# Kernel optimization log

Hardware: AMD Instinct MI355X
Metric: run time of the kernel (lower is better)

## Reference

```python
import jax, jax.numpy as jnp
import numpy as np
import math

N_NODES = 100000
N_EDGES = 1600000
IN_FEATS = 64
H_FEATS = 64
NUM_CLASSES = 2
LS_D = [2, 4, 6, 8]
LS_COEFF = [1.0, 1.0, 1.0, 1.0]
K = 4  # polynomial order per conv (len of each theta)


def _chi_theta(d, coeff):
    # Faithful port of calculate_theta_Chi for d > 0: fit chi-square-like
    # density on [0,2] with a degree-3 Chebyshev series, reverse coeffs.
    n = 2 * d
    m = 1.0 / (n / 2 + 1)  # i = n/2 - 1, m = 1/(i+2)
    def y(x):
        x = np.asarray(x, dtype=np.float64)
        return 1.0 / (2 ** (n / 2) * math.gamma(n / 2)) * (x / m) ** (n / 2 - 1) * np.exp(-(x / m) / 2)
    xs = np.linspace(0.0, 2.0, 20001)
    S = np.trapz(y(xs), xs)  # dense trapezoid ~ scipy.integrate.quad on [0,2]
    lambs = np.linspace(0.0, 2.0, 500)
    c = np.polynomial.chebyshev.chebfit(lambs, y(lambs) / S, 3)
    return (c[::-1] * coeff).astype(np.float32)

THETAS_NP = np.stack([_chi_theta(d, c) for d, c in zip(LS_D, LS_COEFF)])  # [4, K]


def setup_inputs() -> dict:
    key = jax.random.key(0)
    ks = jax.random.split(key, 8)
    sc = 0.05
    return {
        "x": jax.random.normal(ks[0], (N_NODES, IN_FEATS), dtype=jnp.float32),
        "src": jax.random.randint(ks[1], (N_EDGES,), 0, N_NODES, dtype=jnp.int32),
        "dst": jax.random.randint(ks[2], (N_EDGES,), 0, N_NODES, dtype=jnp.int32),
        "thetas": jnp.asarray(THETAS_NP),
        "W1": jax.random.normal(ks[3], (IN_FEATS, H_FEATS), dtype=jnp.float32) * sc,
        "b1": jnp.zeros((H_FEATS,), dtype=jnp.float32),
        "W2": jax.random.normal(ks[4], (H_FEATS, H_FEATS), dtype=jnp.float32) * sc,
        "b2": jnp.zeros((H_FEATS,), dtype=jnp.float32),
        "Wm1": jax.random.normal(ks[5], (H_FEATS * len(LS_D), H_FEATS), dtype=jnp.float32) * sc,
        "bm1": jnp.zeros((H_FEATS,), dtype=jnp.float32),
        "Wm2": jax.random.normal(ks[6], (H_FEATS, NUM_CLASSES), dtype=jnp.float32) * sc,
        "bm2": jnp.zeros((NUM_CLASSES,), dtype=jnp.float32),
    }


def reference(x, src, dst, thetas, W1, b1, W2, b2, Wm1, bm1, Wm2, bm2):
    n = x.shape[0]
    # input MLP stem
    h = jax.nn.relu(x @ W1 + b1)
    h = jax.nn.relu(h @ W2 + b2)
    # D^{-1/2} from in-degrees (clamped to >= 1), as in DGL in_degrees()
    deg = jax.ops.segment_sum(jnp.ones_like(dst, dtype=h.dtype), dst, num_segments=n)
    dinv = jnp.maximum(deg, 1.0) ** -0.5  # [N]
    dinv = dinv[:, None]  # [N, 1]
    # shared Laplacian power sequence: feats[k] = L^k h with L = I - D^-1/2 A D^-1/2
    feats = [h]
    f = h
    for _ in range(K - 1):
        t = f * dinv                                   # [N, H]
        agg = jax.ops.segment_sum(t[src], dst, num_segments=n)  # gather-scatter SpMM
        f = f - agg * dinv
        feats.append(f)
    F = jnp.stack(feats)  # [K, N, H]
    # per-conv polynomial combination, then concat along feature dim
    h_final = jnp.einsum('ck,knh->nch', thetas, F).reshape(n, -1)  # [N, C*H]
    # output MLP (2 layers)
    h_out = jax.nn.relu(h_final @ Wm1 + bm1)
    return h_out @ Wm2 + bm2
```

## Files before the change

kernel.cpp:

```cpp
#include <hip/hip_runtime.h>
#include <math.h>

#define TS  256
#define GS  192
#define BCAP2 4608
#define CHUNK 4096

typedef __attribute__((ext_vector_type(8))) short short8v;
typedef __attribute__((ext_vector_type(4))) float f32x4;

__device__ __forceinline__ unsigned short f2bf(float f) {
    unsigned int u = __builtin_bit_cast(unsigned int, f);
    u += 0x7fff + ((u >> 16) & 1);
    return (unsigned short)(u >> 16);
}
__device__ __forceinline__ float bf2f(unsigned short s) {
    return __builtin_bit_cast(float, ((unsigned int)s) << 16);
}
__device__ __forceinline__ void fma4(float4& a, float s, const float4& b) {
    a.x = fmaf(s, b.x, a.x);
    a.y = fmaf(s, b.y, a.y);
    a.z = fmaf(s, b.z, a.z);
    a.w = fmaf(s, b.w, a.w);
}

__global__ void zero_k(int* __restrict__ p, int n) {
    int i = blockIdx.x * blockDim.x + threadIdx.x;
    int st = gridDim.x * blockDim.x;
    for (; i < n; i += st) p[i] = 0;
}

__global__ __launch_bounds__(256) void part1_k(const int* __restrict__ src,
        const int* __restrict__ dst, int* __restrict__ gcnt,
        unsigned int* __restrict__ pairs, int E, int NB) {
    __shared__ int lcnt[512];
    __shared__ int lbase[512];
    __shared__ int lpos[512];
    int tid = threadIdx.x;
    int base = blockIdx.x * CHUNK;
    int m = E - base; if (m > CHUNK) m = CHUNK;
    for (int b = tid; b < NB; b += 256) { lcnt[b] = 0; lpos[b] = 0; }
    __syncthreads();
    for (int i = tid; i < m; i += 256)
        atomicAdd(&lcnt[dst[base + i] >> 8], 1);
    __syncthreads();
    for (int b = tid; b < NB; b += 256)
        lbase[b] = (lcnt[b] > 0) ? atomicAdd(&gcnt[b], lcnt[b]) : 0;
    __syncthreads();
    for (int i = tid; i < m; i += 256) {
        int s = src[base + i], d = dst[base + i];
        int b = d >> 8;
        int p = atomicAdd(&lpos[b], 1);
        int idx = lbase[b] + p;
        if (idx < BCAP2)
            pairs[(size_t)b * BCAP2 + idx] = (unsigned int)s | ((unsigned int)(d & 255) << 17);
    }
}

__global__ __launch_bounds__(512) void bscan_k(const int* __restrict__ gcnt,
        int* __restrict__ bbase, int* __restrict__ rowp, int NB, int E, int n) {
    __shared__ int buf[512];
    int tid = threadIdx.x;
    int v = (tid < NB) ? (gcnt[tid] > BCAP2 ? BCAP2 : gcnt[tid]) : 0;
    buf[tid] = v;
    __syncthreads();
    int x = v;
    for (int off = 1; off < 512; off <<= 1) {
        int t = (tid >= off) ? buf[tid - off] : 0;
        __syncthreads();
        x += t;
        buf[tid] = x;
        __syncthreads();
    }
    if (tid < NB) bbase[tid] = x - v;
    if (tid == 0) rowp[n] = E;
}

__global__ __launch_bounds__(256) void csr2_k(const int* __restrict__ gcnt,
        const unsigned int* __restrict__ pairs, const int* __restrict__ bbase,
        int* __restrict__ rowp, int* __restrict__ colb, float* __restrict__ dinv, int n) {
    int b = blockIdx.x;
    int tid = threadIdx.x;
    int cntb = gcnt[b]; if (cntb > BCAP2) cntb = BCAP2;
    const unsigned int* pb = pairs + (size_t)b * BCAP2;
    __shared__ int c[256];
    __shared__ int sc[256];
    __shared__ int lpos[256];
    c[tid] = 0; lpos[tid] = 0;
    __syncthreads();
    for (int i = tid; i < cntb; i += 256)
        atomicAdd(&c[pb[i] >> 17], 1);
    __syncthreads();
    int v = c[tid];
    sc[tid] = v;
    __syncthreads();
    int x = v;
    for (int off = 1; off < 256; off <<= 1) {
        int t = (tid >= off) ? sc[tid - off] : 0;
        __syncthreads();
        x += t;
        sc[tid] = x;
        __syncthreads();
    }
    int ex = x - v;
    sc[tid] = ex;
    int node = b * 256 + tid;
    if (node < n) {
        rowp[node] = bbase[b] + ex;
        dinv[node] = 1.0f / sqrtf((float)(v > 1 ? v : 1));
    }
    __syncthreads();
    for (int i = tid; i < cntb; i += 256) {
        unsigned int pk = pb[i];
        int j = pk >> 17;
        int p = atomicAdd(&lpos[j], 1);
        colb[bbase[b] + sc[j] + p] = (int)(pk & 0x1FFFF);
    }
}

__global__ __launch_bounds__(256) void mlp_k(const float* __restrict__ x,
        const float* __restrict__ W1, const float* __restrict__ b1,
        const float* __restrict__ W2, const float* __restrict__ b2,
        const float* __restrict__ dinv,
        unsigned short* __restrict__ Ghi, unsigned short* __restrict__ Glo,
        int n, int ntiles) {
    __shared__ float Ws1[64 * 64];
    __shared__ float Ws2[64 * 64];
    __shared__ float xT[64 * 68];
    int tid = threadIdx.x;
    int ti = tid >> 4, tj = tid & 15;
    for (int idx = tid; idx < 4096; idx += 256) { Ws1[idx] = W1[idx]; Ws2[idx] = W2[idx]; }
    float4 b1v = *(const float4*)&b1[4 * tj];
    float4 b2v = *(const float4*)&b2[4 * tj];

    for (int g = blockIdx.x; g < ntiles; g += gridDim.x) {
        int base = g * 64;
        __syncthreads();
        for (int it = 0; it < 4; it++) {
            int node = ti + it * 16;
            int gn = base + node;
            float4 v = make_float4(0.f, 0.f, 0.f, 0.f);
            if (gn < n) v = *(const float4*)&x[(size_t)gn * 64 + 4 * tj];
            xT[(4 * tj + 0) * 68 + node] = v.x;
            xT[(4 * tj + 1) * 68 + node] = v.y;
            xT[(4 * tj + 2) * 68 + node] = v.z;
            xT[(4 * tj + 3) * 68 + node] = v.w;
        }
        __syncthreads();

        float4 a0 = b1v, a1 = b1v, a2 = b1v, a3 = b1v;
        #pragma unroll 8
        for (int k = 0; k < 64; k++) {
            float4 xv = *(const float4*)&xT[k * 68 + 4 * ti];
            float4 wv = *(const float4*)&Ws1[k * 64 + 4 * tj];
            fma4(a0, xv.x, wv); fma4(a1, xv.y, wv); fma4(a2, xv.z, wv); fma4(a3, xv.w, wv);
        }
        __syncthreads();
        {
            int hb = (4 * tj) * 68 + 4 * ti;
            xT[hb + 0 * 68 + 0] = fmaxf(a0.x, 0.f);
            xT[hb + 1 * 68 + 0] = fmaxf(a0.y, 0.f);
            xT[hb + 2 * 68 + 0] = fmaxf(a0.z, 0.f);
            xT[hb + 3 * 68 + 0] = fmaxf(a0.w, 0.f);
            xT[hb + 0 * 68 + 1] = fmaxf(a1.x, 0.f);
            xT[hb + 1 * 68 + 1] = fmaxf(a1.y, 0.f);
            xT[hb + 2 * 68 + 1] = fmaxf(a1.z, 0.f);
            xT[hb + 3 * 68 + 1] = fmaxf(a1.w, 0.f);
            xT[hb + 0 * 68 + 2] = fmaxf(a2.x, 0.f);
            xT[hb + 1 * 68 + 2] = fmaxf(a2.y, 0.f);
            xT[hb + 2 * 68 + 2] = fmaxf(a2.z, 0.f);
            xT[hb + 3 * 68 + 2] = fmaxf(a2.w, 0.f);
            xT[hb + 0 * 68 + 3] = fmaxf(a3.x, 0.f);
            xT[hb + 1 * 68 + 3] = fmaxf(a3.y, 0.f);
            xT[hb + 2 * 68 + 3] = fmaxf(a3.z, 0.f);
            xT[hb + 3 * 68 + 3] = fmaxf(a3.w, 0.f);
        }
        __syncthreads();

        a0 = b2v; a1 = b2v; a2 = b2v; a3 = b2v;
        #pragma unroll 8
        for (int k = 0; k < 64; k++) {
            float4 xv = *(const float4*)&xT[k * 68 + 4 * ti];
            float4 wv = *(const float4*)&Ws2[k * 64 + 4 * tj];
            fma4(a0, xv.x, wv); fma4(a1, xv.y, wv); fma4(a2, xv.z, wv); fma4(a3, xv.w, wv);
        }
        int gn0 = base + 4 * ti;
#define STORE_ROW(ai, ii)                                                                  \
        {                                                                                  \
            int gn = gn0 + (ii);                                                           \
            if (gn < n) {                                                                  \
                float dg = dinv[gn];                                                       \
                float g0 = fmaxf(ai.x, 0.f) * dg, g1 = fmaxf(ai.y, 0.f) * dg;              \
                float g2 = fmaxf(ai.z, 0.f) * dg, g3 = fmaxf(ai.w, 0.f) * dg;              \
                ushort4 hv, lv;                                                            \
                hv.x = f2bf(g0); lv.x = f2bf(g0 - bf2f(hv.x));                             \
                hv.y = f2bf(g1); lv.y = f2bf(g1 - bf2f(hv.y));                             \
                hv.z = f2bf(g2); lv.z = f2bf(g2 - bf2f(hv.z));                             \
                hv.w = f2bf(g3); lv.w = f2bf(g3 - bf2f(hv.w));                             \
                *(ushort4*)&Ghi[(size_t)gn * TS + 4 * tj] = hv;                            \
                *(ushort4*)&Glo[(size_t)gn * GS + 4 * tj] = lv;                            \
            }                                                                              \
        }
        STORE_ROW(a0, 0) STORE_ROW(a1, 1) STORE_ROW(a2, 2) STORE_ROW(a3, 3)
#undef STORE_ROW
    }
}

__global__ void wm1p_k(const float* __restrict__ thetas, const float* __restrict__ Wm1,
                       unsigned short* __restrict__ Wth, unsigned short* __restrict__ Wtl) {
    int idx = blockIdx.x * blockDim.x + threadIdx.x;
    if (idx >= 16384) return;
    int j = idx & 63;
    int q = idx >> 6;
    int k = q >> 6;
    int hh = q & 63;
    float a = 0.f;
    for (int c = 0; c < 4; c++) a += thetas[c * 4 + k] * Wm1[(c * 64 + hh) * 64 + j];
    unsigned short hi = f2bf(a);
    float r = a - bf2f(hi);
    Wth[j * 256 + q] = hi;
    Wtl[j * 256 + q] = f2bf(r);
}

__global__ __launch_bounds__(256) void prop_k(
        const unsigned short* __restrict__ TinHi,
        const unsigned short* __restrict__ TinLo,
        unsigned short* __restrict__ ToutHi,
        unsigned short* __restrict__ ToutLo,
        const int* __restrict__ rowp, const int* __restrict__ colb,
        const float* __restrict__ dinv, int n, int writeLo) {
    int w = (blockIdx.x * blockDim.x + threadIdx.x) >> 6;
    int lane = threadIdx.x & 63;
    int nA = 2 * w, nB = 2 * w + 1;
    if (nA >= n) return;
    bool hasB = (nB < n);
    int eA = rowp[nA], endA = rowp[nA + 1];
    int eB = 0, endB = 0;
    if (hasB) { eB = rowp[nB]; endB = rowp[nB + 1]; }
    float a0 = 0.f, a1 = 0.f, b0 = 0.f, b1 = 0.f;
    while (eA + 7 < endA && eB + 7 < endB) {
        int sA0 = colb[eA],     sA1 = colb[eA + 1], sA2 = colb[eA + 2], sA3 = colb[eA + 3];
        int sA4 = colb[eA + 4], sA5 = colb[eA + 5], sA6 = colb[eA + 6], sA7 = colb[eA + 7];
        int sB0 = colb[eB],     sB1 = colb[eB + 1], sB2 = colb[eB + 2], sB3 = colb[eB + 3];
        int sB4 = colb[eB + 4], sB5 = colb[eB + 5], sB6 = colb[eB + 6], sB7 = colb[eB + 7];
        float fA0 = bf2f(TinHi[(size_t)sA0 * TS + lane]);
        float fA1 = bf2f(TinHi[(size_t)sA1 * TS + lane]);
        float fA2 = bf2f(TinHi[(size_t)sA2 * TS + lane]);
        float fA3 = bf2f(TinHi[(size_t)sA3 * TS + lane]);
        float fA4 = bf2f(TinHi[(size_t)sA4 * TS + lane]);
        float fA5 = bf2f(TinHi[(size_t)sA5 * TS + lane]);
        float fA6 = bf2f(TinHi[(size_t)sA6 * TS + lane]);
        float fA7 = bf2f(TinHi[(size_t)sA7 * TS + lane]);
        float fB0 = bf2f(TinHi[(size_t)sB0 * TS + lane]);
        float fB1 = bf2f(TinHi[(size_t)sB1 * TS + lane]);
        float fB2 = bf2f(TinHi[(size_t)sB2 * TS + lane]);
        float fB3 = bf2f(TinHi[(size_t)sB3 * TS + lane]);
        float fB4 = bf2f(TinHi[(size_t)sB4 * TS + lane]);
        float fB5 = bf2f(TinHi[(size_t)sB5 * TS + lane]);
        float fB6 = bf2f(TinHi[(size_t)sB6 * TS + lane]);
        float fB7 = bf2f(TinHi[(size_t)sB7 * TS + lane]);
        a0 += (fA0 + fA2) + (fA4 + fA6);
        a1 += (fA1 + fA3) + (fA5 + fA7);
        b0 += (fB0 + fB2) + (fB4 + fB6);
        b1 += (fB1 + fB3) + (fB5 + fB7);
        eA += 8; eB += 8;
    }
    while (eA + 3 < endA) {
        int s0 = colb[eA], s1 = colb[eA + 1], s2 = colb[eA + 2], s3 = colb[eA + 3];
        float f0 = bf2f(TinHi[(size_t)s0 * TS + lane]);
        float f1 = bf2f(TinHi[(size_t)s1 * TS + lane]);
        float f2 = bf2f(TinHi[(size_t)s2 * TS + lane]);
        float f3 = bf2f(TinHi[(size_t)s3 * TS + lane]);
        a0 += f0 + f2; a1 += f1 + f3;
        eA += 4;
    }
    while (eB + 3 < endB) {
        int s0 = colb[eB], s1 = colb[eB + 1], s2 = colb[eB + 2], s3 = colb[eB + 3];
        float f0 = bf2f(TinHi[(size_t)s0 * TS + lane]);
        float f1 = bf2f(TinHi[(size_t)s1 * TS + lane]);
        float f2 = bf2f(TinHi[(size_t)s2 * TS + lane]);
        float f3 = bf2f(TinHi[(size_t)s3 * TS + lane]);
        b0 += f0 + f2; b1 += f1 + f3;
        eB += 4;
    }
    for (; eA < endA; ++eA) a0 += bf2f(TinHi[(size_t)colb[eA] * TS + lane]);
    for (; eB < endB; ++eB) b0 += bf2f(TinHi[(size_t)colb[eB] * TS + lane]);

    {
        float acc = a0 + a1;
        float dg = dinv[nA];
        float gin = bf2f(TinHi[(size_t)nA * TS + lane]) + bf2f(TinLo[(size_t)nA * GS + lane]);
        float go = gin - dg * dg * acc;
        unsigned short hi = f2bf(go);
        ToutHi[(size_t)nA * TS + lane] = hi;
        if (writeLo) ToutLo[(size_t)nA * GS + lane] = f2bf(go - bf2f(hi));
    }
    if (hasB) {
        float acc = b0 + b1;
        float dg = dinv[nB];
        float gin = bf2f(TinHi[(size_t)nB * TS + lane]) + bf2f(TinLo[(size_t)nB * GS + lane]);
        float go = gin - dg * dg * acc;
        unsigned short hi = f2bf(go);
        ToutHi[(size_t)nB * TS + lane] = hi;
        if (writeLo) ToutLo[(size_t)nB * GS + lane] = f2bf(go - bf2f(hi));
    }
}

__global__ __launch_bounds__(512) void final_k(const unsigned short* __restrict__ Ghi,
        const float* __restrict__ dinv,
        const unsigned short* __restrict__ Wth, const unsigned short* __restrict__ Wtl,
        const float* __restrict__ bm1, const float* __restrict__ Wm2,
        const float* __restrict__ bm2, float* __restrict__ out, int n, int ntiles) {
    __shared__ unsigned short Bs[32768];
    __shared__ unsigned short As[32768];
    __shared__ float Lp[4][128][2];
    int tid = threadIdx.x;
    int w = tid >> 6, l = tid & 63;
    int cw = w & 3, half = w >> 2;
    int colg = 16 * cw + (l & 15);
    int grp = l >> 4;

    for (int i = tid; i < 4096; i += 512) {
        int byte = i * 16;
        int col = byte >> 9;
        int swz = byte ^ ((col & 7) << 4);
        uint4 v = (byte < 32768) ? *(const uint4*)((const char*)Wth + byte)
                                 : *(const uint4*)((const char*)Wtl + (byte - 32768));
        *(uint4*)((char*)Bs + swz) = v;
    }
    float bm1c = bm1[colg];
    float w2x = Wm2[colg * 2 + 0], w2y = Wm2[colg * 2 + 1];
    float bo0 = bm2[0], bo1 = bm2[1];
    __syncthreads();

    for (int g = blockIdx.x; g < ntiles; g += gridDim.x) {
        const char* asrc = (const char*)(Ghi + (size_t)g * 128 * TS);
        for (int i = tid; i < 4096; i += 512) {
            int byte = i * 16;
            int row = byte >> 9;
            int swz = byte ^ ((row & 7) << 4);
            *(uint4*)((char*)As + swz) = *(const uint4*)(asrc + byte);
        }
        __syncthreads();

        for (int rt = 0; rt < 4; rt++) {
            int arow = half * 64 + rt * 16 + (l & 15);
            int abase = arow * 512 + grp * 16;
            int axor = (arow & 7) << 4;
            int bbase = colg * 512 + grp * 16;
            int bxor = (colg & 7) << 4;
            f32x4 acc = {0.f, 0.f, 0.f, 0.f};
            #pragma unroll
            for (int ks = 0; ks < 8; ks++) {
                short8v a  = *(const short8v*)((const char*)As + ((abase + ks * 64) ^ axor));
                int bb = (bbase + ks * 64) ^ bxor;
                short8v bh = *(const short8v*)((const char*)Bs + bb);
                short8v bl = *(const short8v*)((const char*)Bs + (bb + 32768));
                acc = __builtin_amdgcn_mfma_f32_16x16x32_bf16(a, bh, acc, 0, 0, 0);
                acc = __builtin_amdgcn_mfma_f32_16x16x32_bf16(a, bl, acc, 0, 0, 0);
            }
            #pragma unroll
            for (int i = 0; i < 4; i++) {
                int rl = half * 64 + rt * 16 + (l >> 4) * 4 + i;
                int grow = g * 128 + rl;
                float s = (grow < n) ? (1.0f / dinv[grow]) : 0.f;
                float h = fmaxf(fmaf(acc[i], s, bm1c), 0.f);
                float q0 = h * w2x, q1 = h * w2y;
                q0 += __shfl_xor(q0, 1); q1 += __shfl_xor(q1, 1);
                q0 += __shfl_xor(q0, 2); q1 += __shfl_xor(q1, 2);
                q0 += __shfl_xor(q0, 4); q1 += __shfl_xor(q1, 4);
                q0 += __shfl_xor(q0, 8); q1 += __shfl_xor(q1, 8);
                if ((l & 15) == 0) {
                    Lp[cw][rl][0] = q0;
                    Lp[cw][rl][1] = q1;
                }
            }
        }
        __syncthreads();
        if (tid < 256) {
            int r = tid >> 1, ch = tid & 1;
            int grow = g * 128 + r;
            if (grow < n) {
                float v = Lp[0][r][ch] + Lp[1][r][ch] + Lp[2][r][ch] + Lp[3][r][ch]
                        + ((ch == 0) ? bo0 : bo1);
                out[grow * 2 + ch] = v;
            }
        }
    }
}

extern "C" void kernel_launch(void* const* d_in, const int* in_sizes, int n_in,
                              void* d_out, int out_size, void* d_ws, size_t ws_size,
                              hipStream_t stream) {
    const float* x      = (const float*)d_in[0];
    const int*   src    = (const int*)d_in[1];
    const int*   dst    = (const int*)d_in[2];
    const float* thetas = (const float*)d_in[3];
    const float* W1     = (const float*)d_in[4];
    const float* b1     = (const float*)d_in[5];
    const float* W2     = (const float*)d_in[6];
    const float* b2     = (const float*)d_in[7];
    const float* Wm1    = (const float*)d_in[8];
    const float* bm1    = (const float*)d_in[9];
    const float* Wm2    = (const float*)d_in[10];
    const float* bm2    = (const float*)d_in[11];
    float* out = (float*)d_out;

    int n = in_sizes[0] / 64;
    int E = in_sizes[1];
    int ntiles  = (n + 63) / 64;
    int ntiles2 = (n + 127) / 128;
    int NB = (n + 255) / 256;

    unsigned short* Glo = (unsigned short*)d_ws;
    float* dinv  = (float*)(Glo + (size_t)n * GS);
    int*   rowp  = (int*)(dinv + n);
    int*   colb  = rowp + (n + 1);
    size_t woff = (((size_t)(colb + E) - (size_t)d_ws) + 15) & ~(size_t)15;
    unsigned short* Wth = (unsigned short*)((char*)d_ws + woff);
    unsigned short* Wtl = Wth + 16384;
    int*   gcnt  = (int*)(Wtl + 16384);
    int*   bbase = gcnt + NB;
    size_t uoff = (((size_t)(bbase + NB) - (size_t)d_ws) + 255) & ~(size_t)255;
    unsigned int*   pairs = (unsigned int*)((char*)d_ws + uoff);
    unsigned short* Ghi   = (unsigned short*)pairs;

    int nchunksP = (E + CHUNK - 1) / CHUNK;

    zero_k<<<4, 256, 0, stream>>>(gcnt, NB);
    part1_k<<<nchunksP, 256, 0, stream>>>(src, dst, gcnt, pairs, E, NB);
    bscan_k<<<1, 512, 0, stream>>>(gcnt, bbase, rowp, NB, E, n);
    csr2_k<<<NB, 256, 0, stream>>>(gcnt, pairs, bbase, rowp, colb, dinv, n);

    mlp_k<<<768, 256, 0, stream>>>(x, W1, b1, W2, b2, dinv, Ghi, Glo, n, ntiles);
    wm1p_k<<<64, 256, 0, stream>>>(thetas, Wm1, Wth, Wtl);

    int nwaves = (n + 1) / 2;
    int pblocks = ((size_t)nwaves * 64 + 255) / 256;
    prop_k<<<pblocks, 256, 0, stream>>>(
        Ghi + 0 * 64, Glo + 0 * 64, Ghi + 1 * 64, Glo + 1 * 64, rowp, colb, dinv, n, 1);
    prop_k<<<pblocks, 256, 0, stream>>>(
        Ghi + 1 * 64, Glo + 1 * 64, Ghi + 2 * 64, Glo + 2 * 64, rowp, colb, dinv, n, 1);
    prop_k<<<pblocks, 256, 0, stream>>>(
        Ghi + 2 * 64, Glo + 2 * 64, Ghi + 3 * 64, Glo + 2 * 64, rowp, colb, dinv, n, 0);

    int fgrid = ntiles2 < 256 ? ntiles2 : 256;
    final_k<<<fgrid, 512, 0, stream>>>(Ghi, dinv, Wth, Wtl, bm1, Wm2, bm2, out, n, ntiles2);
}
```

Measured before the change: 277.3 us.

## Use split-bf16 MFMA for input MLP and drop the bucket scan kernel

The input MLP moves from scalar FP32 FMAs in LDS to bf16 MFMA 16x16x32 with hi/lo split operands (three MFMAs per step), using swizzled LDS tiles and weights pre-transposed by the extended wm1p kernel. The bucket prefix-scan kernel is replaced by an atomic running total in csr2_k, so bucket order becomes arbitrary. rowp now packs the start offset and degree into one word, so prop_k reads one value per node instead of two. The zeroing kernel becomes a memset. The split-bf16 scheme drops the lo*lo term, which slightly changes precision.

```diff
diff --git a/kernel.cpp b/kernel.cpp
--- a/kernel.cpp
+++ b/kernel.cpp
@@ -16,18 +16,6 @@
 }
 __device__ __forceinline__ float bf2f(unsigned short s) {
     return __builtin_bit_cast(float, ((unsigned int)s) << 16);
-}
-__device__ __forceinline__ void fma4(float4& a, float s, const float4& b) {
-    a.x = fmaf(s, b.x, a.x);
-    a.y = fmaf(s, b.y, a.y);
-    a.z = fmaf(s, b.z, a.z);
-    a.w = fmaf(s, b.w, a.w);
-}
-
-__global__ void zero_k(int* __restrict__ p, int n) {
-    int i = blockIdx.x * blockDim.x + threadIdx.x;
-    int st = gridDim.x * blockDim.x;
-    for (; i < n; i += st) p[i] = 0;
 }
 
 __global__ __launch_bounds__(256) void part1_k(const int* __restrict__ src,
@@ -57,28 +45,10 @@
     }
 }
 
-__global__ __launch_bounds__(512) void bscan_k(const int* __restrict__ gcnt,
-        int* __restrict__ bbase, int* __restrict__ rowp, int NB, int E, int n) {
-    __shared__ int buf[512];
-    int tid = threadIdx.x;
-    int v = (tid < NB) ? (gcnt[tid] > BCAP2 ? BCAP2 : gcnt[tid]) : 0;
-    buf[tid] = v;
-    __syncthreads();
-    int x = v;
-    for (int off = 1; off < 512; off <<= 1) {
-        int t = (tid >= off) ? buf[tid - off] : 0;
-        __syncthreads();
-        x += t;
-        buf[tid] = x;
-        __syncthreads();
-    }
-    if (tid < NB) bbase[tid] = x - v;
-    if (tid == 0) rowp[n] = E;
-}
-
 __global__ __launch_bounds__(256) void csr2_k(const int* __restrict__ gcnt,
-        const unsigned int* __restrict__ pairs, const int* __restrict__ bbase,
-        int* __restrict__ rowp, int* __restrict__ colb, float* __restrict__ dinv, int n) {
+        int* __restrict__ gtot, const unsigned int* __restrict__ pairs,
+        unsigned int* __restrict__ rowp, int* __restrict__ colb,
+        float* __restrict__ dinv, int n) {
     int b = blockIdx.x;
     int tid = threadIdx.x;
     int cntb = gcnt[b]; if (cntb > BCAP2) cntb = BCAP2;
@@ -86,6 +56,8 @@
     __shared__ int c[256];
     __shared__ int sc[256];
     __shared__ int lpos[256];
+    __shared__ int sbase;
+    if (tid == 0) sbase = atomicAdd(gtot, cntb);
     c[tid] = 0; lpos[tid] = 0;
     __syncthreads();
     for (int i = tid; i < cntb; i += 256)
@@ -104,9 +76,10 @@
     }
     int ex = x - v;
     sc[tid] = ex;
+    int bbase = sbase;
     int node = b * 256 + tid;
     if (node < n) {
-        rowp[node] = bbase[b] + ex;
+        rowp[node] = (unsigned int)(bbase + ex) | ((unsigned int)v << 21);
         dinv[node] = 1.0f / sqrtf((float)(v > 1 ? v : 1));
     }
     __syncthreads();
@@ -114,112 +87,179 @@
         unsigned int pk = pb[i];
         int j = pk >> 17;
         int p = atomicAdd(&lpos[j], 1);
-        colb[bbase[b] + sc[j] + p] = (int)(pk & 0x1FFFF);
+        colb[bbase + sc[j] + p] = (int)(pk & 0x1FFFF);
+    }
+}
+
+__global__ void wm1p_k(const float* __restrict__ thetas, const float* __restrict__ Wm1,
+                       const float* __restrict__ W1, const float* __restrict__ W2,
+                       unsigned short* __restrict__ Wth, unsigned short* __restrict__ Wtl,
+                       unsigned short* __restrict__ W1th, unsigned short* __restrict__ W1tl,
+                       unsigned short* __restrict__ W2th, unsigned short* __restrict__ W2tl) {
+    int idx = blockIdx.x * blockDim.x + threadIdx.x;
+    if (idx < 16384) {
+        int j = idx & 63;
+        int q = idx >> 6;
+        int k = q >> 6;
+        int hh = q & 63;
+        float a = 0.f;
+        for (int c = 0; c < 4; c++) a += thetas[c * 4 + k] * Wm1[(c * 64 + hh) * 64 + j];
+        unsigned short hi = f2bf(a);
+        Wth[j * 256 + q] = hi;
+        Wtl[j * 256 + q] = f2bf(a - bf2f(hi));
+    } else if (idx < 24576) {
+        int t = idx - 16384;
+        const float* W = (t < 4096) ? W1 : W2;
+        unsigned short* Th = (t < 4096) ? W1th : W2th;
+        unsigned short* Tl = (t < 4096) ? W1tl : W2tl;
+        int u = t & 4095;
+        int j = u >> 6, k = u & 63;
+        float a = W[k * 64 + j];
+        unsigned short hi = f2bf(a);
+        Th[u] = hi;
+        Tl[u] = f2bf(a - bf2f(hi));
     }
 }
 
 __global__ __launch_bounds__(256) void mlp_k(const float* __restrict__ x,
-        const float* __restrict__ W1, const float* __restrict__ b1,
-        const float* __restrict__ W2, const float* __restrict__ b2,
+        const unsigned short* __restrict__ W1th, const unsigned short* __restrict__ W1tl,
+        const unsigned short* __restrict__ W2th, const unsigned short* __restrict__ W2tl,
+        const float* __restrict__ b1, const float* __restrict__ b2,
         const float* __restrict__ dinv,
         unsigned short* __restrict__ Ghi, unsigned short* __restrict__ Glo,
         int n, int ntiles) {
-    __shared__ float Ws1[64 * 64];
-    __shared__ float Ws2[64 * 64];
-    __shared__ float xT[64 * 68];
+    __shared__ __align__(16) unsigned short B1h[4096], B1l[4096], B2h[4096], B2l[4096];
+    __shared__ __align__(16) unsigned short Ah[4][1024], Al[4][1024];
     int tid = threadIdx.x;
-    int ti = tid >> 4, tj = tid & 15;
-    for (int idx = tid; idx < 4096; idx += 256) { Ws1[idx] = W1[idx]; Ws2[idx] = W2[idx]; }
-    float4 b1v = *(const float4*)&b1[4 * tj];
-    float4 b2v = *(const float4*)&b2[4 * tj];
+    int w = tid >> 6, l = tid & 63;
+    int lr = l & 15, grp = l >> 4;
+
+    for (int i = tid; i < 512; i += 256) {
+        int byte = i * 16;
+        int col = byte >> 7;
+        int swz = byte ^ ((col & 7) << 4);
+        *(uint4*)((char*)B1h + swz) = *(const uint4*)((const char*)W1th + byte);
+        *(uint4*)((char*)B1l + swz) = *(const uint4*)((const char*)W1tl + byte);
+        *(uint4*)((char*)B2h + swz) = *(const uint4*)((const char*)W2th + byte);
+        *(uint4*)((char*)B2l + swz) = *(const uint4*)((const char*)W2tl + byte);
+    }
+    float b1v[4], b2v[4];
+    #pragma unroll
+    for (int cb = 0; cb < 4; cb++) {
+        b1v[cb] = b1[cb * 16 + lr];
+        b2v[cb] = b2[cb * 16 + lr];
+    }
+    __syncthreads();
+
+    unsigned short* ah = Ah[w];
+    unsigned short* al = Al[w];
 
     for (int g = blockIdx.x; g < ntiles; g += gridDim.x) {
-        int base = g * 64;
-        __syncthreads();
+        int row0 = g * 64 + w * 16;
+        #pragma unroll
         for (int it = 0; it < 4; it++) {
-            int node = ti + it * 16;
-            int gn = base + node;
+            int chunk = it * 64 + l;
+            int r = chunk >> 4;
+            int cc = (chunk & 15) * 4;
+            int gn = row0 + r;
             float4 v = make_float4(0.f, 0.f, 0.f, 0.f);
-            if (gn < n) v = *(const float4*)&x[(size_t)gn * 64 + 4 * tj];
-            xT[(4 * tj + 0) * 68 + node] = v.x;
-            xT[(4 * tj + 1) * 68 + node] = v.y;
-            xT[(4 * tj + 2) * 68 + node] = v.z;
-            xT[(4 * tj + 3) * 68 + node] = v.w;
-        }
-        __syncthreads();
-
-        float4 a0 = b1v, a1 = b1v, a2 = b1v, a3 = b1v;
-        #pragma unroll 8
-        for (int k = 0; k < 64; k++) {
-            float4 xv = *(const float4*)&xT[k * 68 + 4 * ti];
-            float4 wv = *(const float4*)&Ws1[k * 64 + 4 * tj];
-            fma4(a0, xv.x, wv); fma4(a1, xv.y, wv); fma4(a2, xv.z, wv); fma4(a3, xv.w, wv);
-        }
-        __syncthreads();
-        {
-            int hb = (4 * tj) * 68 + 4 * ti;
-            xT[hb + 0 * 68 + 0] = fmaxf(a0.x, 0.f);
-            xT[hb + 1 * 68 + 0] = fmaxf(a0.y, 0.f);
-            xT[hb + 2 * 68 + 0] = fmaxf(a0.z, 0.f);
-            xT[hb + 3 * 68 + 0] = fmaxf(a0.w, 0.f);
-            xT[hb + 0 * 68 + 1] = fmaxf(a1.x, 0.f);
-            xT[hb + 1 * 68 + 1] = fmaxf(a1.y, 0.f);
-            xT[hb + 2 * 68 + 1] = fmaxf(a1.z, 0.f);
-            xT[hb + 3 * 68 + 1] = fmaxf(a1.w, 0.f);
-            xT[hb + 0 * 68 + 2] = fmaxf(a2.x, 0.f);
-            xT[hb + 1 * 68 + 2] = fmaxf(a2.y, 0.f);
-            xT[hb + 2 * 68 + 2] = fmaxf(a2.z, 0.f);
-            xT[hb + 3 * 68 + 2] = fmaxf(a2.w, 0.f);
-            xT[hb + 0 * 68 + 3] = fmaxf(a3.x, 0.f);
-            xT[hb + 1 * 68 + 3] = fmaxf(a3.y, 0.f);
-            xT[hb + 2 * 68 + 3] = fmaxf(a3.z, 0.f);
-            xT[hb + 3 * 68 + 3] = fmaxf(a3.w, 0.f);
-        }
-        __syncthreads();
-
-        a0 = b2v; a1 = b2v; a2 = b2v; a3 = b2v;
-        #pragma unroll 8
-        for (int k = 0; k < 64; k++) {
-            float4 xv = *(const float4*)&xT[k * 68 + 4 * ti];
-            float4 wv = *(const float4*)&Ws2[k * 64 + 4 * tj];
-            fma4(a0, xv.x, wv); fma4(a1, xv.y, wv); fma4(a2, xv.z, wv); fma4(a3, xv.w, wv);
-        }
-        int gn0 = base + 4 * ti;
-#define STORE_ROW(ai, ii)                                                                  \
-        {                                                                                  \
-            int gn = gn0 + (ii);                                                           \
-            if (gn < n) {                                                                  \
-                float dg = dinv[gn];                                                       \
-                float g0 = fmaxf(ai.x, 0.f) * dg, g1 = fmaxf(ai.y, 0.f) * dg;              \
-                float g2 = fmaxf(ai.z, 0.f) * dg, g3 = fmaxf(ai.w, 0.f) * dg;              \
-                ushort4 hv, lv;                                                            \
-                hv.x = f2bf(g0); lv.x = f2bf(g0 - bf2f(hv.x));                             \
-                hv.y = f2bf(g1); lv.y = f2bf(g1 - bf2f(hv.y));                             \
-                hv.z = f2bf(g2); lv.z = f2bf(g2 - bf2f(hv.z));                             \
-                hv.w = f2bf(g3); lv.w = f2bf(g3 - bf2f(hv.w));                             \
-                *(ushort4*)&Ghi[(size_t)gn * TS + 4 * tj] = hv;                            \
-                *(ushort4*)&Glo[(size_t)gn * GS + 4 * tj] = lv;                            \
-            }                                                                              \
-        }
-        STORE_ROW(a0, 0) STORE_ROW(a1, 1) STORE_ROW(a2, 2) STORE_ROW(a3, 3)
-#undef STORE_ROW
-    }
-}
-
-__global__ void wm1p_k(const float* __restrict__ thetas, const float* __restrict__ Wm1,
-                       unsigned short* __restrict__ Wth, unsigned short* __restrict__ Wtl) {
-    int idx = blockIdx.x * blockDim.x + threadIdx.x;
-    if (idx >= 16384) return;
-    int j = idx & 63;
-    int q = idx >> 6;
-    int k = q >> 6;
-    int hh = q & 63;
-    float a = 0.f;
-    for (int c = 0; c < 4; c++) a += thetas[c * 4 + k] * Wm1[(c * 64 + hh) * 64 + j];
-    unsigned short hi = f2bf(a);
-    float r = a - bf2f(hi);
-    Wth[j * 256 + q] = hi;
-    Wtl[j * 256 + q] = f2bf(r);
+            if (gn < n) v = *(const float4*)&x[(size_t)gn * 64 + cc];
+            ushort4 hv, lv;
+            hv.x = f2bf(v.x); lv.x = f2bf(v.x - bf2f(hv.x));
+            hv.y = f2bf(v.y); lv.y = f2bf(v.y - bf2f(hv.y));
+            hv.z = f2bf(v.z); lv.z = f2bf(v.z - bf2f(hv.z));
+            hv.w = f2bf(v.w); lv.w = f2bf(v.w - bf2f(hv.w));
+            int byte = (r * 128 + cc * 2) ^ ((r & 7) << 4);
+            *(ushort4*)((char*)ah + byte) = hv;
+            *(ushort4*)((char*)al + byte) = lv;
+        }
+        f32x4 acc1[4];
+        #pragma unroll
+        for (int cb = 0; cb < 4; cb++) {
+            f32x4 acc = {0.f, 0.f, 0.f, 0.f};
+            #pragma unroll
+            for (int ks = 0; ks < 2; ks++) {
+                int ko = (ks * 32 + grp * 8) * 2;
+                int abyte = (lr * 128 + ko) ^ ((lr & 7) << 4);
+                short8v a_h = *(const short8v*)((const char*)ah + abyte);
+                short8v a_l = *(const short8v*)((const char*)al + abyte);
+                int col = cb * 16 + lr;
+                int bbyte = (col * 128 + ko) ^ ((col & 7) << 4);
+                short8v b_h = *(const short8v*)((const char*)B1h + bbyte);
+                short8v b_l = *(const short8v*)((const char*)B1l + bbyte);
+                acc = __builtin_amdgcn_mfma_f32_16x16x32_bf16(a_h, b_h, acc, 0, 0, 0);
+                acc = __builtin_amdgcn_mfma_f32_16x16x32_bf16(a_h, b_l, acc, 0, 0, 0);
+                acc = __builtin_amdgcn_mfma_f32_16x16x32_bf16(a_l, b_h, acc, 0, 0, 0);
+            }
+            acc1[cb] = acc;
+        }
+        #pragma unroll
+        for (int cb = 0; cb < 4; cb++) {
+            int col = cb * 16 + lr;
+            #pragma unroll
+            for (int i = 0; i < 4; i++) {
+                int r = grp * 4 + i;
+                float h = fmaxf(acc1[cb][i] + b1v[cb], 0.f);
+                unsigned short hi = f2bf(h);
+                int byte = (r * 128 + col * 2) ^ ((r & 7) << 4);
+                *(unsigned short*)((char*)ah + byte) = hi;
+                *(unsigned short*)((char*)al + byte) = f2bf(h - bf2f(hi));
+            }
+        }
+        f32x4 acc2[4];
+        #pragma unroll
+        for (int cb = 0; cb < 4; cb++) {
+            f32x4 acc = {0.f, 0.f, 0.f, 0.f};
+            #pragma unroll
+            for (int ks = 0; ks < 2; ks++) {
+                int ko = (ks * 32 + grp * 8) * 2;
+                int abyte = (lr * 128 + ko) ^ ((lr & 7) << 4);
+                short8v a_h = *(const short8v*)((const char*)ah + abyte);
+                short8v a_l = *(const short8v*)((const char*)al + abyte);
+                int col = cb * 16 + lr;
+                int bbyte = (col * 128 + ko) ^ ((col & 7) << 4);
+                short8v b_h = *(const short8v*)((const char*)B2h + bbyte);
+                short8v b_l = *(const short8v*)((const char*)B2l + bbyte);
+                acc = __builtin_amdgcn_mfma_f32_16x16x32_bf16(a_h, b_h, acc, 0, 0, 0);
+                acc = __builtin_amdgcn_mfma_f32_16x16x32_bf16(a_h, b_l, acc, 0, 0, 0);
+                acc = __builtin_amdgcn_mfma_f32_16x16x32_bf16(a_l, b_h, acc, 0, 0, 0);
+            }
+            acc2[cb] = acc;
+        }
+        float dgv[4];
+        #pragma unroll
+        for (int i = 0; i < 4; i++) {
+            int gn = row0 + grp * 4 + i;
+            dgv[i] = (gn < n) ? dinv[gn] : 0.f;
+        }
+        #pragma unroll
+        for (int cb = 0; cb < 4; cb++) {
+            int col = cb * 16 + lr;
+            #pragma unroll
+            for (int i = 0; i < 4; i++) {
+                int r = grp * 4 + i;
+                float gq = fmaxf(acc2[cb][i] + b2v[cb], 0.f) * dgv[i];
+                unsigned short hi = f2bf(gq);
+                int byte = (r * 128 + col * 2) ^ ((r & 7) << 4);
+                *(unsigned short*)((char*)ah + byte) = hi;
+                *(unsigned short*)((char*)al + byte) = f2bf(gq - bf2f(hi));
+            }
+        }
+        #pragma unroll
+        for (int it = 0; it < 2; it++) {
+            int gidx = it * 64 + l;
+            int r = gidx >> 3;
+            int go = (gidx & 7) * 16;
+            int gn = row0 + r;
+            if (gn < n) {
+                int byte = (r * 128 + go) ^ ((r & 7) << 4);
+                uint4 hv = *(const uint4*)((const char*)ah + byte);
+                uint4 lv = *(const uint4*)((const char*)al + byte);
+                *(uint4*)((char*)&Ghi[(size_t)gn * TS] + go) = hv;
+                *(uint4*)((char*)&Glo[(size_t)gn * GS] + go) = lv;
+            }
+        }
+    }
 }
 
 __global__ __launch_bounds__(256) void prop_k(
@@ -227,16 +267,20 @@
         const unsigned short* __restrict__ TinLo,
         unsigned short* __restrict__ ToutHi,
         unsigned short* __restrict__ ToutLo,
-        const int* __restrict__ rowp, const int* __restrict__ colb,
+        const unsigned int* __restrict__ rowp, const int* __restrict__ colb,
         const float* __restrict__ dinv, int n, int writeLo) {
     int w = (blockIdx.x * blockDim.x + threadIdx.x) >> 6;
     int lane = threadIdx.x & 63;
     int nA = 2 * w, nB = 2 * w + 1;
     if (nA >= n) return;
     bool hasB = (nB < n);
-    int eA = rowp[nA], endA = rowp[nA + 1];
+    unsigned int pA = rowp[nA];
+    int eA = (int)(pA & 0x1FFFFF), endA = eA + (int)(pA >> 21);
     int eB = 0, endB = 0;
-    if (hasB) { eB = rowp[nB]; endB = rowp[nB + 1]; }
+    if (hasB) {
+        unsigned int pB = rowp[nB];
+        eB = (int)(pB & 0x1FFFFF); endB = eB + (int)(pB >> 21);
+    }
     float a0 = 0.f, a1 = 0.f, b0 = 0.f, b1 = 0.f;
     while (eA + 7 < endA && eB + 7 < endB) {
         int sA0 = colb[eA],     sA1 = colb[eA + 1], sA2 = colb[eA + 2], sA3 = colb[eA + 3];
@@ -413,27 +457,30 @@
     int NB = (n + 255) / 256;
 
     unsigned short* Glo = (unsigned short*)d_ws;
-    float* dinv  = (float*)(Glo + (size_t)n * GS);
-    int*   rowp  = (int*)(dinv + n);
-    int*   colb  = rowp + (n + 1);
+    float* dinv = (float*)(Glo + (size_t)n * GS);
+    unsigned int* rowp = (unsigned int*)(dinv + n);
+    int* colb = (int*)(rowp + n);
     size_t woff = (((size_t)(colb + E) - (size_t)d_ws) + 15) & ~(size_t)15;
-    unsigned short* Wth = (unsigned short*)((char*)d_ws + woff);
-    unsigned short* Wtl = Wth + 16384;
-    int*   gcnt  = (int*)(Wtl + 16384);
-    int*   bbase = gcnt + NB;
-    size_t uoff = (((size_t)(bbase + NB) - (size_t)d_ws) + 255) & ~(size_t)255;
+    unsigned short* Wth  = (unsigned short*)((char*)d_ws + woff);
+    unsigned short* Wtl  = Wth + 16384;
+    unsigned short* W1th = Wtl + 16384;
+    unsigned short* W1tl = W1th + 4096;
+    unsigned short* W2th = W1tl + 4096;
+    unsigned short* W2tl = W2th + 4096;
+    int* gcnt = (int*)(W2tl + 4096);
+    int* gtot = gcnt + NB;
+    size_t uoff = (((size_t)(gtot + 1) - (size_t)d_ws) + 255) & ~(size_t)255;
     unsigned int*   pairs = (unsigned int*)((char*)d_ws + uoff);
     unsigned short* Ghi   = (unsigned short*)pairs;
 
     int nchunksP = (E + CHUNK - 1) / CHUNK;
 
-    zero_k<<<4, 256, 0, stream>>>(gcnt, NB);
+    hipMemsetAsync(gcnt, 0, (size_t)(NB + 1) * sizeof(int), stream);
     part1_k<<<nchunksP, 256, 0, stream>>>(src, dst, gcnt, pairs, E, NB);
-    bscan_k<<<1, 512, 0, stream>>>(gcnt, bbase, rowp, NB, E, n);
-    csr2_k<<<NB, 256, 0, stream>>>(gcnt, pairs, bbase, rowp, colb, dinv, n);
-
-    mlp_k<<<768, 256, 0, stream>>>(x, W1, b1, W2, b2, dinv, Ghi, Glo, n, ntiles);
-    wm1p_k<<<64, 256, 0, stream>>>(thetas, Wm1, Wth, Wtl);
+    csr2_k<<<NB, 256, 0, stream>>>(gcnt, gtot, pairs, rowp, colb, dinv, n);
+    wm1p_k<<<96, 256, 0, stream>>>(thetas, Wm1, W1, W2, Wth, Wtl, W1th, W1tl, W2th, W2tl);
+
+    mlp_k<<<512, 256, 0, stream>>>(x, W1th, W1tl, W2th, W2tl, b1, b2, dinv, Ghi, Glo, n, ntiles);
 
     int nwaves = (n + 1) / 2;
     int pblocks = ((size_t)nwaves * 64 + 255) / 256;
```

After: 278.2 us. No clear change (+0.3%).
